# Optimization experiments

Measured on AMD Instinct MI355X. Metric: run time of the kernel, lower is better.

Reference implementation:

```python
import jax, jax.numpy as jnp
import numpy as np
import math

B, T, C = 2, 2048, 768
NH, HD = 12, 64  # n_head, head_dim

def setup_inputs() -> dict:
    key = jax.random.key(0)
    k1, k2, k3 = jax.random.split(key, 3)
    x = jax.random.normal(k1, (B, T, C), dtype=jnp.float32)
    mask = jnp.tril(jnp.ones((T, T), dtype=bool))[None, None]  # [1,1,T,T] causal
    Wqkv = jax.random.normal(k2, (C, 3 * C), dtype=jnp.float32) * (1.0 / math.sqrt(C))
    Wproj = jax.random.normal(k3, (C, C), dtype=jnp.float32) * (1.0 / math.sqrt(C))
    return {"x": x, "mask": mask, "Wqkv": Wqkv, "Wproj": Wproj}

def reference(x, mask, Wqkv, Wproj):
    b, t, c = x.shape
    qkv = x @ Wqkv  # [b,t,3c]
    q, k, v = jnp.split(qkv, 3, axis=-1)
    q = q.reshape(b, t, NH, HD).transpose(0, 2, 1, 3)  # [b,h,t,d]
    k = k.reshape(b, t, NH, HD).transpose(0, 2, 1, 3)
    v = v.reshape(b, t, NH, HD).transpose(0, 2, 1, 3)
    att = jnp.einsum('bhqd,bhkd->bhqk', q, k) / math.sqrt(HD)
    att = jnp.where(mask, att, -jnp.inf)
    att = jax.nn.softmax(att, axis=-1)
    out = jnp.einsum('bhqk,bhkd->bhqd', att, v)
    out = out.transpose(0, 2, 1, 3).reshape(b, t, c)
    return out @ Wproj
```

## Files before the change

### kernel.cpp

```cpp
#include <hip/hip_runtime.h>
#include <hip/hip_bf16.h>

#define T_   2048
#define C_   768
#define NH_  12
#define HD_  64
#define M_   (2*T_)
#define N1_  (3*C_)
#define PB_  ((size_t)NH_*T_*HD_)
#define KS_  0.180336880f
#define MK_  8.65617024f

typedef __attribute__((ext_vector_type(8))) short  short8;
typedef __attribute__((ext_vector_type(4))) short  shortx4;
typedef __attribute__((ext_vector_type(4))) float  floatx4;

__device__ __forceinline__ floatx4 mfma_bf16(short8 a, short8 b, floatx4 c) {
    return __builtin_amdgcn_mfma_f32_16x16x32_bf16(a, b, c, 0, 0, 0);
}
__device__ __forceinline__ float fast_exp2(float x) {
    return __builtin_amdgcn_exp2f(x);
}

__global__ __launch_bounds__(256) void prep1(const float* __restrict__ x,
                                             const float* __restrict__ wqkv,
                                             __hip_bfloat16* __restrict__ xb,
                                             __hip_bfloat16* __restrict__ wqkvT) {
    if (blockIdx.x < 3072) {
        const int idx = blockIdx.x * 256 + threadIdx.x;
        const floatx4 v = ((const floatx4*)x)[idx];
        union { __hip_bfloat16 h[4]; shortx4 s; } u;
#pragma unroll
        for (int j = 0; j < 4; j++) u.h[j] = __float2bfloat16(v[j]);
        ((shortx4*)xb)[idx] = u.s;
    } else {
        const int j  = (blockIdx.x - 3072) * 256 + threadIdx.x;
        const int k8 = j / N1_;
        const int n  = j - k8 * N1_;
        union { __hip_bfloat16 h[8]; short8 s; } u;
#pragma unroll
        for (int jj = 0; jj < 8; jj++)
            u.h[jj] = __float2bfloat16(wqkv[(size_t)(k8 * 8 + jj) * N1_ + n]);
        *(short8*)(wqkvT + (size_t)n * C_ + k8 * 8) = u.s;
    }
}

__global__ __launch_bounds__(256) void prep2(const float* __restrict__ wproj,
                                             __hip_bfloat16* __restrict__ wprojT) {
    const int j  = blockIdx.x * 256 + threadIdx.x;
    const int k8 = j / C_;
    const int n  = j - k8 * C_;
    union { __hip_bfloat16 h[8]; short8 s; } u;
#pragma unroll
    for (int jj = 0; jj < 8; jj++)
        u.h[jj] = __float2bfloat16(wproj[(size_t)(k8 * 8 + jj) * C_ + n]);
    *(short8*)(wprojT + (size_t)n * C_ + k8 * 8) = u.s;
}

__global__ __launch_bounds__(256) void gemm_bt128(const __hip_bfloat16* __restrict__ A,
                                                  const __hip_bfloat16* __restrict__ Bt,
                                                  int N, int K, int mode,
                                                  void* __restrict__ O0,
                                                  __hip_bfloat16* __restrict__ O1,
                                                  __hip_bfloat16* __restrict__ O2) {
    __shared__ __align__(16) __hip_bfloat16 As[128 * 40];
    __shared__ __align__(16) __hip_bfloat16 Bs[128 * 40];

    const int tid  = threadIdx.x;
    const int n0   = blockIdx.x * 128;
    const int m0   = blockIdx.y * 128;
    const int srow = tid >> 1;
    const int scol = (tid & 1) * 16;
    const int wave = tid >> 6;
    const int ln   = tid & 63;
    const int l16  = ln & 15;
    const int q4   = ln >> 4;
    const int wm   = (wave >> 1) * 64;
    const int wn   = (wave & 1) * 64;

    floatx4 acc[4][4];
#pragma unroll
    for (int i = 0; i < 4; i++)
#pragma unroll
        for (int j = 0; j < 4; j++) acc[i][j] = (floatx4){0.f, 0.f, 0.f, 0.f};

    const __hip_bfloat16* Ap = A  + (size_t)(m0 + srow) * K + scol;
    const __hip_bfloat16* Bp = Bt + (size_t)(n0 + srow) * K + scol;

    for (int k0 = 0; k0 < K; k0 += 32) {
        short8 a0 = *(const short8*)(Ap + k0);
        short8 a1 = *(const short8*)(Ap + k0 + 8);
        short8 b0 = *(const short8*)(Bp + k0);
        short8 b1 = *(const short8*)(Bp + k0 + 8);
        __syncthreads();
        *(short8*)(As + srow * 40 + scol)     = a0;
        *(short8*)(As + srow * 40 + scol + 8) = a1;
        *(short8*)(Bs + srow * 40 + scol)     = b0;
        *(short8*)(Bs + srow * 40 + scol + 8) = b1;
        __syncthreads();
        short8 af[4], bfr[4];
#pragma unroll
        for (int i = 0; i < 4; i++) {
            af[i]  = *(const short8*)(As + (wm + i * 16 + l16) * 40 + q4 * 8);
            bfr[i] = *(const short8*)(Bs + (wn + i * 16 + l16) * 40 + q4 * 8);
        }
#pragma unroll
        for (int i = 0; i < 4; i++)
#pragma unroll
            for (int j = 0; j < 4; j++)
                acc[i][j] = mfma_bf16(af[i], bfr[j], acc[i][j]);
    }

#pragma unroll
    for (int i = 0; i < 4; i++) {
        const int mbase = m0 + wm + i * 16 + q4 * 4;
#pragma unroll
        for (int j = 0; j < 4; j++) {
            const int n = n0 + wn + j * 16 + l16;
#pragma unroll
            for (int r = 0; r < 4; r++) {
                const int mm = mbase + r;
                const float fv = acc[i][j][r];
                if (mode == 1) {
                    ((float*)O0)[(size_t)mm * N + n] = fv;
                } else {
                    const __hip_bfloat16 hv = __float2bfloat16(fv);
                    const int which = n / C_;
                    const int rem   = n - which * C_;
                    const int h     = rem >> 6;
                    const int d     = rem & 63;
                    const int bh    = (mm >> 11) * NH_ + h;
                    const int t     = mm & (T_ - 1);
                    if (which == 0)      ((__hip_bfloat16*)O0)[((size_t)bh * T_ + t) * HD_ + d] = hv;
                    else if (which == 1) O1[((size_t)bh * T_ + t) * HD_ + d] = hv;
                    else                 O2[((size_t)bh * HD_ + d) * T_ + t] = hv;
                }
            }
        }
    }
}

__global__ __launch_bounds__(256) void gemm_bt64(const __hip_bfloat16* __restrict__ A,
                                                 const __hip_bfloat16* __restrict__ Bt,
                                                 int N, int K,
                                                 float* __restrict__ O0) {
    __shared__ __align__(16) __hip_bfloat16 As[64 * 40];
    __shared__ __align__(16) __hip_bfloat16 Bs[64 * 40];

    const int tid  = threadIdx.x;
    const int n0   = blockIdx.x * 64;
    const int m0   = blockIdx.y * 64;
    const int srow = tid >> 2;
    const int scol = (tid & 3) * 8;
    const int wave = tid >> 6;
    const int ln   = tid & 63;
    const int l16  = ln & 15;
    const int q4   = ln >> 4;
    const int wm   = (wave >> 1) * 32;
    const int wn   = (wave & 1) * 32;

    floatx4 acc[2][2];
#pragma unroll
    for (int i = 0; i < 2; i++)
#pragma unroll
        for (int j = 0; j < 2; j++) acc[i][j] = (floatx4){0.f, 0.f, 0.f, 0.f};

    const __hip_bfloat16* Ap = A  + (size_t)(m0 + srow) * K + scol;
    const __hip_bfloat16* Bp = Bt + (size_t)(n0 + srow) * K + scol;

    for (int k0 = 0; k0 < K; k0 += 32) {
        short8 av = *(const short8*)(Ap + k0);
        short8 bv = *(const short8*)(Bp + k0);
        __syncthreads();
        *(short8*)(As + srow * 40 + scol) = av;
        *(short8*)(Bs + srow * 40 + scol) = bv;
        __syncthreads();
        short8 af[2], bfr[2];
#pragma unroll
        for (int i = 0; i < 2; i++) {
            af[i]  = *(const short8*)(As + (wm + i * 16 + l16) * 40 + q4 * 8);
            bfr[i] = *(const short8*)(Bs + (wn + i * 16 + l16) * 40 + q4 * 8);
        }
#pragma unroll
        for (int i = 0; i < 2; i++)
#pragma unroll
            for (int j = 0; j < 2; j++)
                acc[i][j] = mfma_bf16(af[i], bfr[j], acc[i][j]);
    }

#pragma unroll
    for (int i = 0; i < 2; i++) {
        const int mbase = m0 + wm + i * 16 + q4 * 4;
#pragma unroll
        for (int j = 0; j < 2; j++) {
            const int n = n0 + wn + j * 16 + l16;
#pragma unroll
            for (int r = 0; r < 4; r++)
                O0[(size_t)(mbase + r) * N + n] = acc[i][j][r];
        }
    }
}

__global__ __launch_bounds__(256) void gemm_xw(const void* __restrict__ A,
                                               const float* __restrict__ Bf,
                                               int a_is_f32, int row0, int N, int K,
                                               int mode, int orow0,
                                               void* __restrict__ O0,
                                               __hip_bfloat16* __restrict__ O1,
                                               __hip_bfloat16* __restrict__ O2) {
    __shared__ __align__(16) __hip_bfloat16 As[128 * 40];
    __shared__ __align__(16) __hip_bfloat16 Bs[128 * 40];

    const int tid  = threadIdx.x;
    const int n0   = blockIdx.x * 128;
    const int m0   = blockIdx.y * 128;
    const int srow = tid >> 1;
    const int scol = (tid & 1) * 16;
    const int bn   = tid & 127;
    const int bg   = tid >> 7;
    const int wave = tid >> 6;
    const int ln   = tid & 63;
    const int l16  = ln & 15;
    const int q4   = ln >> 4;
    const int wm   = (wave >> 1) * 64;
    const int wn   = (wave & 1) * 64;

    floatx4 acc[4][4];
#pragma unroll
    for (int i = 0; i < 4; i++)
#pragma unroll
        for (int j = 0; j < 4; j++) acc[i][j] = (floatx4){0.f, 0.f, 0.f, 0.f};

    const size_t arow = (size_t)(row0 + m0 + srow) * K;

    for (int k0 = 0; k0 < K; k0 += 32) {
        union { __hip_bfloat16 h[16]; short8 v[2]; } au, bu;
        if (a_is_f32) {
            const float* Af = (const float*)A;
            const size_t base = arow + k0 + scol;
            floatx4 f0 = *(const floatx4*)(Af + base);
            floatx4 f1 = *(const floatx4*)(Af + base + 4);
            floatx4 f2 = *(const floatx4*)(Af + base + 8);
            floatx4 f3 = *(const floatx4*)(Af + base + 12);
#pragma unroll
            for (int j = 0; j < 4; j++) {
                au.h[j]      = __float2bfloat16(f0[j]);
                au.h[4 + j]  = __float2bfloat16(f1[j]);
                au.h[8 + j]  = __float2bfloat16(f2[j]);
                au.h[12 + j] = __float2bfloat16(f3[j]);
            }
        } else {
            const __hip_bfloat16* Ab = (const __hip_bfloat16*)A;
            au.v[0] = *(const short8*)(Ab + arow + k0 + scol);
            au.v[1] = *(const short8*)(Ab + arow + k0 + scol + 8);
        }
#pragma unroll
        for (int j = 0; j < 16; j++)
            bu.h[j] = __float2bfloat16(Bf[(size_t)(k0 + bg * 16 + j) * N + n0 + bn]);
        __syncthreads();
        *(short8*)(As + srow * 40 + scol)      = au.v[0];
        *(short8*)(As + srow * 40 + scol + 8)  = au.v[1];
        *(short8*)(Bs + bn * 40 + bg * 16)     = bu.v[0];
        *(short8*)(Bs + bn * 40 + bg * 16 + 8) = bu.v[1];
        __syncthreads();
        short8 af[4], bfr[4];
#pragma unroll
        for (int i = 0; i < 4; i++) {
            af[i]  = *(const short8*)(As + (wm + i * 16 + l16) * 40 + q4 * 8);
            bfr[i] = *(const short8*)(Bs + (wn + i * 16 + l16) * 40 + q4 * 8);
        }
#pragma unroll
        for (int i = 0; i < 4; i++)
#pragma unroll
            for (int j = 0; j < 4; j++)
                acc[i][j] = mfma_bf16(af[i], bfr[j], acc[i][j]);
    }

#pragma unroll
    for (int i = 0; i < 4; i++) {
        const int mbase = m0 + wm + i * 16 + q4 * 4;
#pragma unroll
        for (int j = 0; j < 4; j++) {
            const int n = n0 + wn + j * 16 + l16;
#pragma unroll
            for (int r = 0; r < 4; r++) {
                const int mm = mbase + r;
                const float fv = acc[i][j][r];
                if (mode == 1) {
                    ((float*)O0)[(size_t)(orow0 + mm) * N + n] = fv;
                } else {
                    const __hip_bfloat16 hv = __float2bfloat16(fv);
                    const int which = n / C_;
                    const int rem   = n - which * C_;
                    const int h     = rem >> 6;
                    const int d     = rem & 63;
                    const int bh    = (mm >> 11) * NH_ + h;
                    const int t     = mm & (T_ - 1);
                    if (which == 0)      ((__hip_bfloat16*)O0)[((size_t)bh * T_ + t) * HD_ + d] = hv;
                    else if (which == 1) O1[((size_t)bh * T_ + t) * HD_ + d] = hv;
                    else                 O2[((size_t)bh * HD_ + d) * T_ + t] = hv;
                }
            }
        }
    }
}

__global__ __launch_bounds__(256) void attn_fused(const __hip_bfloat16* __restrict__ Q,
                                                  const __hip_bfloat16* __restrict__ Kd,
                                                  const __hip_bfloat16* __restrict__ Vt,
                                                  __hip_bfloat16* __restrict__ O) {
    __shared__ __align__(16) __hip_bfloat16 plds[4][2][16][72];

    const int bh   = blockIdx.x;
    const int wid  = threadIdx.x >> 6;
    const int lane = threadIdx.x & 63;
    const int l16  = lane & 15;
    const int q4   = lane >> 4;
    const int i    = 63 - (int)blockIdx.y;
    const int q0A  = 32 * i;
    const int q0B  = 32 * i + 16;
    const int nch  = (i >> 1) + 1;

    const __hip_bfloat16* Qh = Q  + (size_t)bh * T_ * HD_;
    const __hip_bfloat16* Kh = Kd + (size_t)bh * T_ * HD_;
    const __hip_bfloat16* Vh = Vt + (size_t)bh * HD_ * T_;

    short8 aqA[2], aqB[2];
#pragma unroll
    for (int kt = 0; kt < 2; kt++) {
        aqA[kt] = *(const short8*)(Qh + (size_t)(q0A + l16) * HD_ + kt * 32 + q4 * 8);
        aqB[kt] = *(const short8*)(Qh + (size_t)(q0B + l16) * HD_ + kt * 32 + q4 * 8);
    }

    floatx4 accA[4], accB[4];
#pragma unroll
    for (int ct = 0; ct < 4; ct++) {
        accA[ct] = (floatx4){0.f, 0.f, 0.f, 0.f};
        accB[ct] = (floatx4){0.f, 0.f, 0.f, 0.f};
    }
    float lsA[4] = {0.f, 0.f, 0.f, 0.f};
    float lsB[4] = {0.f, 0.f, 0.f, 0.f};

    for (int c = wid; c < nch; c += 4) {
        const int kv0 = c * 64;
        const bool diag = (c == nch - 1);

        short8 bk[4][2];
#pragma unroll
        for (int nt = 0; nt < 4; nt++)
#pragma unroll
            for (int kt = 0; kt < 2; kt++)
                bk[nt][kt] = *(const short8*)(Kh + (size_t)(kv0 + nt * 16 + l16) * HD_ + kt * 32 + q4 * 8);

        floatx4 sA[4], sB[4];
#pragma unroll
        for (int nt = 0; nt < 4; nt++) {
            sA[nt] = (floatx4){0.f, 0.f, 0.f, 0.f};
            sB[nt] = (floatx4){0.f, 0.f, 0.f, 0.f};
#pragma unroll
            for (int kt = 0; kt < 2; kt++) {
                sA[nt] = mfma_bf16(aqA[kt], bk[nt][kt], sA[nt]);
                sB[nt] = mfma_bf16(aqB[kt], bk[nt][kt], sB[nt]);
            }
        }

        if (diag) {
#pragma unroll
            for (int r = 0; r < 4; r++) {
#pragma unroll
                for (int nt = 0; nt < 4; nt++) {
                    const int kvc = kv0 + nt * 16 + l16;
                    if (kvc > q0A + q4 * 4 + r) sA[nt][r] = -3e38f;
                    if (kvc > q0B + q4 * 4 + r) sB[nt][r] = -3e38f;
                }
            }
        }

#pragma unroll
        for (int r = 0; r < 4; r++) {
            float ra = 0.f, rb = 0.f;
#pragma unroll
            for (int nt = 0; nt < 4; nt++) {
                const float pa = fast_exp2(sA[nt][r] * KS_ - MK_);
                const float pb = fast_exp2(sB[nt][r] * KS_ - MK_);
                plds[wid][0][q4 * 4 + r][nt * 16 + l16] = __float2bfloat16(pa);
                plds[wid][1][q4 * 4 + r][nt * 16 + l16] = __float2bfloat16(pb);
                ra += pa; rb += pb;
            }
            lsA[r] += ra; lsB[r] += rb;
        }

        __threadfence_block();

        short8 apA[2], apB[2];
#pragma unroll
        for (int kt = 0; kt < 2; kt++) {
            apA[kt] = *(const short8*)(&plds[wid][0][l16][kt * 32 + q4 * 8]);
            apB[kt] = *(const short8*)(&plds[wid][1][l16][kt * 32 + q4 * 8]);
        }
#pragma unroll
        for (int ct = 0; ct < 4; ct++)
#pragma unroll
            for (int kt = 0; kt < 2; kt++) {
                short8 bv = *(const short8*)(Vh + (size_t)(ct * 16 + l16) * T_ + kv0 + kt * 32 + q4 * 8);
                accA[ct] = mfma_bf16(apA[kt], bv, accA[ct]);
                accB[ct] = mfma_bf16(apB[kt], bv, accB[ct]);
            }

        __threadfence_block();
    }

#pragma unroll
    for (int off = 1; off < 16; off <<= 1)
#pragma unroll
        for (int r = 0; r < 4; r++) {
            lsA[r] += __shfl_xor(lsA[r], off, 64);
            lsB[r] += __shfl_xor(lsB[r], off, 64);
        }

    __syncthreads();
    floatx4* accbuf = (floatx4*)&plds[0][0][0][0];
    float*   lbuf   = (float*)((char*)&plds[0][0][0][0] + 16384);

    auto publish = [&](int slot) {
#pragma unroll
        for (int ct = 0; ct < 4; ct++) {
            accbuf[((slot * 2 + 0) * 4 + ct) * 64 + lane] = accA[ct];
            accbuf[((slot * 2 + 1) * 4 + ct) * 64 + lane] = accB[ct];
        }
        if (l16 == 0) {
#pragma unroll
            for (int r = 0; r < 4; r++) {
                lbuf[(slot * 2 + 0) * 16 + q4 * 4 + r] = lsA[r];
                lbuf[(slot * 2 + 1) * 16 + q4 * 4 + r] = lsB[r];
            }
        }
    };
    auto mergeIn = [&](int slot) {
#pragma unroll
        for (int ct = 0; ct < 4; ct++) {
            accA[ct] += accbuf[((slot * 2 + 0) * 4 + ct) * 64 + lane];
            accB[ct] += accbuf[((slot * 2 + 1) * 4 + ct) * 64 + lane];
        }
#pragma unroll
        for (int r = 0; r < 4; r++) {
            lsA[r] += lbuf[(slot * 2 + 0) * 16 + q4 * 4 + r];
            lsB[r] += lbuf[(slot * 2 + 1) * 16 + q4 * 4 + r];
        }
    };

    if (wid >= 2) publish(wid - 2);
    __syncthreads();
    if (wid < 2) mergeIn(wid);
    __syncthreads();
    if (wid == 1) publish(0);
    __syncthreads();
    if (wid == 0) {
        mergeIn(0);
        const int orow0 = (bh / NH_) * T_;
        const int hcol  = (bh % NH_) * HD_;
#pragma unroll
        for (int r = 0; r < 4; r++) {
            const float invA = 1.0f / lsA[r];
            const float invB = 1.0f / lsB[r];
            __hip_bfloat16* oA = O + (size_t)(orow0 + q0A + q4 * 4 + r) * C_ + hcol;
            __hip_bfloat16* oB = O + (size_t)(orow0 + q0B + q4 * 4 + r) * C_ + hcol;
#pragma unroll
            for (int ct = 0; ct < 4; ct++) {
                oA[ct * 16 + l16] = __float2bfloat16(accA[ct][r] * invA);
                oB[ct * 16 + l16] = __float2bfloat16(accB[ct][r] * invB);
            }
        }
    }
}

extern "C" void kernel_launch(void* const* d_in, const int* in_sizes, int n_in,
                              void* d_out, int out_size, void* d_ws, size_t ws_size,
                              hipStream_t stream) {
    const float *x = nullptr, *wqkv = nullptr, *wproj = nullptr;
    for (int i = 0; i < n_in; i++) {
        const int s = in_sizes[i];
        if (s == M_ * C_ && !x) x = (const float*)d_in[i];
        else if (s == C_ * N1_ && !wqkv) wqkv = (const float*)d_in[i];
        else if (s == C_ * C_ && !wproj) wproj = (const float*)d_in[i];
    }
    float* out = (float*)d_out;
    __hip_bfloat16* ws = (__hip_bfloat16*)d_ws;
    __hip_bfloat16* Vt = (__hip_bfloat16*)d_out;

    const size_t needB = 6 * PB_ * 2;
    if (ws_size >= needB) {
        __hip_bfloat16* Qall   = ws;
        __hip_bfloat16* Kall   = Qall + 2 * PB_;
        __hip_bfloat16* ATT    = Kall + 2 * PB_;
        __hip_bfloat16* xb     = ATT;
        __hip_bfloat16* wqkvT  = (__hip_bfloat16*)d_out + 2 * PB_;
        __hip_bfloat16* wprojT = Qall;
        prep1<<<dim3(3936), 256, 0, stream>>>(x, wqkv, xb, wqkvT);
        gemm_bt128<<<dim3(N1_ / 128, M_ / 128), 256, 0, stream>>>(
            xb, wqkvT, N1_, C_, 0, (void*)Qall, Kall, Vt);
        attn_fused<<<dim3(2 * NH_, 64), 256, 0, stream>>>(Qall, Kall, Vt, ATT);
        prep2<<<dim3(288), 256, 0, stream>>>(wproj, wprojT);
        gemm_bt64<<<dim3(C_ / 64, M_ / 64), 256, 0, stream>>>(ATT, wprojT, C_, C_, out);
    } else {
        __hip_bfloat16* Qb      = ws;
        __hip_bfloat16* Kb      = Qb + PB_;
        __hip_bfloat16* ATTb[2] = {Kb + PB_, Kb + 2 * PB_};
        for (int b = 0; b < 2; b++) {
            __hip_bfloat16* Vtb = Vt + (size_t)b * PB_;
            gemm_xw<<<dim3(N1_ / 128, T_ / 128), 256, 0, stream>>>(
                x, wqkv, 1, b * T_, N1_, C_, 0, 0, (void*)Qb, Kb, Vtb);
            attn_fused<<<dim3(NH_, 64), 256, 0, stream>>>(Qb, Kb, Vtb, ATTb[b]);
        }
        for (int b = 0; b < 2; b++)
            gemm_xw<<<dim3(C_ / 128, T_ / 128), 256, 0, stream>>>(
                ATTb[b], wproj, 0, 0, C_, C_, 1, b * T_, (void*)out, nullptr, nullptr);
    }
}
```

Baseline: 206.1 us.

## Pair causal query tiles per attention block to balance work across blocks

```diff
diff --git a/kernel.cpp b/kernel.cpp
--- a/kernel.cpp
+++ b/kernel.cpp
@@ -20,6 +20,9 @@
 }
 __device__ __forceinline__ float fast_exp2(float x) {
     return __builtin_amdgcn_exp2f(x);
+}
+__device__ __forceinline__ void wave_fence() {
+    __builtin_amdgcn_fence(__ATOMIC_SEQ_CST, "wavefront");
 }
 
 __global__ __launch_bounds__(256) void prep1(const float* __restrict__ x,
@@ -201,179 +204,83 @@
     }
 }
 
-__global__ __launch_bounds__(256) void gemm_xw(const void* __restrict__ A,
-                                               const float* __restrict__ Bf,
-                                               int a_is_f32, int row0, int N, int K,
-                                               int mode, int orow0,
-                                               void* __restrict__ O0,
-                                               __hip_bfloat16* __restrict__ O1,
-                                               __hip_bfloat16* __restrict__ O2) {
-    __shared__ __align__(16) __hip_bfloat16 As[128 * 40];
-    __shared__ __align__(16) __hip_bfloat16 Bs[128 * 40];
-
-    const int tid  = threadIdx.x;
-    const int n0   = blockIdx.x * 128;
-    const int m0   = blockIdx.y * 128;
-    const int srow = tid >> 1;
-    const int scol = (tid & 1) * 16;
-    const int bn   = tid & 127;
-    const int bg   = tid >> 7;
-    const int wave = tid >> 6;
-    const int ln   = tid & 63;
-    const int l16  = ln & 15;
-    const int q4   = ln >> 4;
-    const int wm   = (wave >> 1) * 64;
-    const int wn   = (wave & 1) * 64;
-
-    floatx4 acc[4][4];
-#pragma unroll
-    for (int i = 0; i < 4; i++)
-#pragma unroll
-        for (int j = 0; j < 4; j++) acc[i][j] = (floatx4){0.f, 0.f, 0.f, 0.f};
-
-    const size_t arow = (size_t)(row0 + m0 + srow) * K;
-
-    for (int k0 = 0; k0 < K; k0 += 32) {
-        union { __hip_bfloat16 h[16]; short8 v[2]; } au, bu;
-        if (a_is_f32) {
-            const float* Af = (const float*)A;
-            const size_t base = arow + k0 + scol;
-            floatx4 f0 = *(const floatx4*)(Af + base);
-            floatx4 f1 = *(const floatx4*)(Af + base + 4);
-            floatx4 f2 = *(const floatx4*)(Af + base + 8);
-            floatx4 f3 = *(const floatx4*)(Af + base + 12);
-#pragma unroll
-            for (int j = 0; j < 4; j++) {
-                au.h[j]      = __float2bfloat16(f0[j]);
-                au.h[4 + j]  = __float2bfloat16(f1[j]);
-                au.h[8 + j]  = __float2bfloat16(f2[j]);
-                au.h[12 + j] = __float2bfloat16(f3[j]);
-            }
-        } else {
-            const __hip_bfloat16* Ab = (const __hip_bfloat16*)A;
-            au.v[0] = *(const short8*)(Ab + arow + k0 + scol);
-            au.v[1] = *(const short8*)(Ab + arow + k0 + scol + 8);
-        }
-#pragma unroll
-        for (int j = 0; j < 16; j++)
-            bu.h[j] = __float2bfloat16(Bf[(size_t)(k0 + bg * 16 + j) * N + n0 + bn]);
-        __syncthreads();
-        *(short8*)(As + srow * 40 + scol)      = au.v[0];
-        *(short8*)(As + srow * 40 + scol + 8)  = au.v[1];
-        *(short8*)(Bs + bn * 40 + bg * 16)     = bu.v[0];
-        *(short8*)(Bs + bn * 40 + bg * 16 + 8) = bu.v[1];
-        __syncthreads();
-        short8 af[4], bfr[4];
-#pragma unroll
-        for (int i = 0; i < 4; i++) {
-            af[i]  = *(const short8*)(As + (wm + i * 16 + l16) * 40 + q4 * 8);
-            bfr[i] = *(const short8*)(Bs + (wn + i * 16 + l16) * 40 + q4 * 8);
-        }
-#pragma unroll
-        for (int i = 0; i < 4; i++)
-#pragma unroll
-            for (int j = 0; j < 4; j++)
-                acc[i][j] = mfma_bf16(af[i], bfr[j], acc[i][j]);
-    }
-
-#pragma unroll
-    for (int i = 0; i < 4; i++) {
-        const int mbase = m0 + wm + i * 16 + q4 * 4;
-#pragma unroll
-        for (int j = 0; j < 4; j++) {
-            const int n = n0 + wn + j * 16 + l16;
-#pragma unroll
-            for (int r = 0; r < 4; r++) {
-                const int mm = mbase + r;
-                const float fv = acc[i][j][r];
-                if (mode == 1) {
-                    ((float*)O0)[(size_t)(orow0 + mm) * N + n] = fv;
-                } else {
-                    const __hip_bfloat16 hv = __float2bfloat16(fv);
-                    const int which = n / C_;
-                    const int rem   = n - which * C_;
-                    const int h     = rem >> 6;
-                    const int d     = rem & 63;
-                    const int bh    = (mm >> 11) * NH_ + h;
-                    const int t     = mm & (T_ - 1);
-                    if (which == 0)      ((__hip_bfloat16*)O0)[((size_t)bh * T_ + t) * HD_ + d] = hv;
-                    else if (which == 1) O1[((size_t)bh * T_ + t) * HD_ + d] = hv;
-                    else                 O2[((size_t)bh * HD_ + d) * T_ + t] = hv;
-                }
-            }
-        }
-    }
-}
-
 __global__ __launch_bounds__(256) void attn_fused(const __hip_bfloat16* __restrict__ Q,
                                                   const __hip_bfloat16* __restrict__ Kd,
                                                   const __hip_bfloat16* __restrict__ Vt,
                                                   __hip_bfloat16* __restrict__ O) {
-    __shared__ __align__(16) __hip_bfloat16 plds[4][2][16][72];
+    __shared__ __align__(16) char smem[33792];
 
     const int bh   = blockIdx.x;
+    const int j    = blockIdx.y;
     const int wid  = threadIdx.x >> 6;
     const int lane = threadIdx.x & 63;
     const int l16  = lane & 15;
     const int q4   = lane >> 4;
-    const int i    = 63 - (int)blockIdx.y;
-    const int q0A  = 32 * i;
-    const int q0B  = 32 * i + 16;
-    const int nch  = (i >> 1) + 1;
+    const int i0   = j;
+    const int i1   = 63 - j;
+    const int nch0 = (i0 >> 1) + 1;
+    const int nch1 = (i1 >> 1) + 1;
+    const int q0[4] = {32 * i0, 32 * i0 + 16, 32 * i1, 32 * i1 + 16};
+
+    auto plds = (__hip_bfloat16(*)[2][16][72])smem;
 
     const __hip_bfloat16* Qh = Q  + (size_t)bh * T_ * HD_;
     const __hip_bfloat16* Kh = Kd + (size_t)bh * T_ * HD_;
     const __hip_bfloat16* Vh = Vt + (size_t)bh * HD_ * T_;
 
-    short8 aqA[2], aqB[2];
-#pragma unroll
-    for (int kt = 0; kt < 2; kt++) {
-        aqA[kt] = *(const short8*)(Qh + (size_t)(q0A + l16) * HD_ + kt * 32 + q4 * 8);
-        aqB[kt] = *(const short8*)(Qh + (size_t)(q0B + l16) * HD_ + kt * 32 + q4 * 8);
-    }
-
-    floatx4 accA[4], accB[4];
+    short8 aq[4][2];
+#pragma unroll
+    for (int t = 0; t < 4; t++)
+#pragma unroll
+        for (int kt = 0; kt < 2; kt++)
+            aq[t][kt] = *(const short8*)(Qh + (size_t)(q0[t] + l16) * HD_ + kt * 32 + q4 * 8);
+
+    floatx4 acc0A[4], acc0B[4], acc1A[4], acc1B[4];
 #pragma unroll
     for (int ct = 0; ct < 4; ct++) {
-        accA[ct] = (floatx4){0.f, 0.f, 0.f, 0.f};
-        accB[ct] = (floatx4){0.f, 0.f, 0.f, 0.f};
-    }
-    float lsA[4] = {0.f, 0.f, 0.f, 0.f};
-    float lsB[4] = {0.f, 0.f, 0.f, 0.f};
-
-    for (int c = wid; c < nch; c += 4) {
-        const int kv0 = c * 64;
-        const bool diag = (c == nch - 1);
-
-        short8 bk[4][2];
-#pragma unroll
-        for (int nt = 0; nt < 4; nt++)
-#pragma unroll
-            for (int kt = 0; kt < 2; kt++)
-                bk[nt][kt] = *(const short8*)(Kh + (size_t)(kv0 + nt * 16 + l16) * HD_ + kt * 32 + q4 * 8);
-
+        acc0A[ct] = (floatx4){0.f, 0.f, 0.f, 0.f};
+        acc0B[ct] = (floatx4){0.f, 0.f, 0.f, 0.f};
+        acc1A[ct] = (floatx4){0.f, 0.f, 0.f, 0.f};
+        acc1B[ct] = (floatx4){0.f, 0.f, 0.f, 0.f};
+    }
+    float ls[4][4];
+#pragma unroll
+    for (int t = 0; t < 4; t++)
+#pragma unroll
+        for (int r = 0; r < 4; r++) ls[t][r] = 0.f;
+
+    auto do_chunk = [&](int kv0, bool diag, int q0A, int q0B,
+                        short8 (&aqA)[2], short8 (&aqB)[2],
+                        floatx4 (&accA)[4], floatx4 (&accB)[4],
+                        float (&lsA)[4], float (&lsB)[4]) {
         floatx4 sA[4], sB[4];
 #pragma unroll
         for (int nt = 0; nt < 4; nt++) {
             sA[nt] = (floatx4){0.f, 0.f, 0.f, 0.f};
             sB[nt] = (floatx4){0.f, 0.f, 0.f, 0.f};
-#pragma unroll
-            for (int kt = 0; kt < 2; kt++) {
-                sA[nt] = mfma_bf16(aqA[kt], bk[nt][kt], sA[nt]);
-                sB[nt] = mfma_bf16(aqB[kt], bk[nt][kt], sB[nt]);
+        }
+#pragma unroll
+        for (int kt = 0; kt < 2; kt++) {
+            short8 bk[4];
+#pragma unroll
+            for (int nt = 0; nt < 4; nt++)
+                bk[nt] = *(const short8*)(Kh + (size_t)(kv0 + nt * 16 + l16) * HD_ + kt * 32 + q4 * 8);
+#pragma unroll
+            for (int nt = 0; nt < 4; nt++) {
+                sA[nt] = mfma_bf16(aqA[kt], bk[nt], sA[nt]);
+                sB[nt] = mfma_bf16(aqB[kt], bk[nt], sB[nt]);
             }
         }
 
         if (diag) {
 #pragma unroll
-            for (int r = 0; r < 4; r++) {
+            for (int r = 0; r < 4; r++)
 #pragma unroll
                 for (int nt = 0; nt < 4; nt++) {
                     const int kvc = kv0 + nt * 16 + l16;
                     if (kvc > q0A + q4 * 4 + r) sA[nt][r] = -3e38f;
                     if (kvc > q0B + q4 * 4 + r) sB[nt][r] = -3e38f;
                 }
-            }
         }
 
 #pragma unroll
@@ -390,7 +297,7 @@
             lsA[r] += ra; lsB[r] += rb;
         }
 
-        __threadfence_block();
+        wave_fence();
 
         short8 apA[2], apB[2];
 #pragma unroll
@@ -407,45 +314,55 @@
                 accB[ct] = mfma_bf16(apB[kt], bv, accB[ct]);
             }
 
-        __threadfence_block();
+        wave_fence();
+    };
+
+    for (int t = wid; t < 33; t += 4) {
+        if (t < nch0) {
+            do_chunk(t * 64, t == nch0 - 1, q0[0], q0[1], aq[0], aq[1],
+                     acc0A, acc0B, ls[0], ls[1]);
+        } else {
+            const int c = t - nch0;
+            do_chunk(c * 64, c == nch1 - 1, q0[2], q0[3], aq[2], aq[3],
+                     acc1A, acc1B, ls[2], ls[3]);
+        }
     }
 
 #pragma unroll
     for (int off = 1; off < 16; off <<= 1)
 #pragma unroll
-        for (int r = 0; r < 4; r++) {
-            lsA[r] += __shfl_xor(lsA[r], off, 64);
-            lsB[r] += __shfl_xor(lsB[r], off, 64);
-        }
+        for (int t = 0; t < 4; t++)
+#pragma unroll
+            for (int r = 0; r < 4; r++)
+                ls[t][r] += __shfl_xor(ls[t][r], off, 64);
 
     __syncthreads();
-    floatx4* accbuf = (floatx4*)&plds[0][0][0][0];
-    float*   lbuf   = (float*)((char*)&plds[0][0][0][0] + 16384);
+    floatx4* accbuf = (floatx4*)smem;
+    float*   lbuf   = (float*)(smem + 32768);
 
     auto publish = [&](int slot) {
-#pragma unroll
-        for (int ct = 0; ct < 4; ct++) {
-            accbuf[((slot * 2 + 0) * 4 + ct) * 64 + lane] = accA[ct];
-            accbuf[((slot * 2 + 1) * 4 + ct) * 64 + lane] = accB[ct];
-        }
-        if (l16 == 0) {
-#pragma unroll
-            for (int r = 0; r < 4; r++) {
-                lbuf[(slot * 2 + 0) * 16 + q4 * 4 + r] = lsA[r];
-                lbuf[(slot * 2 + 1) * 16 + q4 * 4 + r] = lsB[r];
-            }
+        floatx4* a[4] = {acc0A, acc0B, acc1A, acc1B};
+#pragma unroll
+        for (int t = 0; t < 4; t++) {
+#pragma unroll
+            for (int ct = 0; ct < 4; ct++)
+                accbuf[(((slot * 4 + t) * 4) + ct) * 64 + lane] = a[t][ct];
+            if (l16 == 0)
+#pragma unroll
+                for (int r = 0; r < 4; r++)
+                    lbuf[(slot * 4 + t) * 16 + q4 * 4 + r] = ls[t][r];
         }
     };
     auto mergeIn = [&](int slot) {
-#pragma unroll
-        for (int ct = 0; ct < 4; ct++) {
-            accA[ct] += accbuf[((slot * 2 + 0) * 4 + ct) * 64 + lane];
-            accB[ct] += accbuf[((slot * 2 + 1) * 4 + ct) * 64 + lane];
-        }
-#pragma unroll
-        for (int r = 0; r < 4; r++) {
-            lsA[r] += lbuf[(slot * 2 + 0) * 16 + q4 * 4 + r];
-            lsB[r] += lbuf[(slot * 2 + 1) * 16 + q4 * 4 + r];
+        floatx4* a[4] = {acc0A, acc0B, acc1A, acc1B};
+#pragma unroll
+        for (int t = 0; t < 4; t++) {
+#pragma unroll
+            for (int ct = 0; ct < 4; ct++)
+                a[t][ct] += accbuf[(((slot * 4 + t) * 4) + ct) * 64 + lane];
+#pragma unroll
+            for (int r = 0; r < 4; r++)
+                ls[t][r] += lbuf[(slot * 4 + t) * 16 + q4 * 4 + r];
         }
     };
 
@@ -459,18 +376,17 @@
         mergeIn(0);
         const int orow0 = (bh / NH_) * T_;
         const int hcol  = (bh % NH_) * HD_;
-#pragma unroll
-        for (int r = 0; r < 4; r++) {
-            const float invA = 1.0f / lsA[r];
-            const float invB = 1.0f / lsB[r];
-            __hip_bfloat16* oA = O + (size_t)(orow0 + q0A + q4 * 4 + r) * C_ + hcol;
-            __hip_bfloat16* oB = O + (size_t)(orow0 + q0B + q4 * 4 + r) * C_ + hcol;
-#pragma unroll
-            for (int ct = 0; ct < 4; ct++) {
-                oA[ct * 16 + l16] = __float2bfloat16(accA[ct][r] * invA);
-                oB[ct * 16 + l16] = __float2bfloat16(accB[ct][r] * invB);
+        floatx4* a[4] = {acc0A, acc0B, acc1A, acc1B};
+#pragma unroll
+        for (int t = 0; t < 4; t++)
+#pragma unroll
+            for (int r = 0; r < 4; r++) {
+                const float inv = 1.0f / ls[t][r];
+                __hip_bfloat16* orow = O + (size_t)(orow0 + q0[t] + q4 * 4 + r) * C_ + hcol;
+#pragma unroll
+                for (int ct = 0; ct < 4; ct++)
+                    orow[ct * 16 + l16] = __float2bfloat16(a[t][ct][r] * inv);
             }
-        }
     }
 }
 
@@ -488,32 +404,16 @@
     __hip_bfloat16* ws = (__hip_bfloat16*)d_ws;
     __hip_bfloat16* Vt = (__hip_bfloat16*)d_out;
 
-    const size_t needB = 6 * PB_ * 2;
-    if (ws_size >= needB) {
-        __hip_bfloat16* Qall   = ws;
-        __hip_bfloat16* Kall   = Qall + 2 * PB_;
-        __hip_bfloat16* ATT    = Kall + 2 * PB_;
-        __hip_bfloat16* xb     = ATT;
-        __hip_bfloat16* wqkvT  = (__hip_bfloat16*)d_out + 2 * PB_;
-        __hip_bfloat16* wprojT = Qall;
-        prep1<<<dim3(3936), 256, 0, stream>>>(x, wqkv, xb, wqkvT);
-        gemm_bt128<<<dim3(N1_ / 128, M_ / 128), 256, 0, stream>>>(
-            xb, wqkvT, N1_, C_, 0, (void*)Qall, Kall, Vt);
-        attn_fused<<<dim3(2 * NH_, 64), 256, 0, stream>>>(Qall, Kall, Vt, ATT);
-        prep2<<<dim3(288), 256, 0, stream>>>(wproj, wprojT);
-        gemm_bt64<<<dim3(C_ / 64, M_ / 64), 256, 0, stream>>>(ATT, wprojT, C_, C_, out);
-    } else {
-        __hip_bfloat16* Qb      = ws;
-        __hip_bfloat16* Kb      = Qb + PB_;
-        __hip_bfloat16* ATTb[2] = {Kb + PB_, Kb + 2 * PB_};
-        for (int b = 0; b < 2; b++) {
-            __hip_bfloat16* Vtb = Vt + (size_t)b * PB_;
-            gemm_xw<<<dim3(N1_ / 128, T_ / 128), 256, 0, stream>>>(
-                x, wqkv, 1, b * T_, N1_, C_, 0, 0, (void*)Qb, Kb, Vtb);
-            attn_fused<<<dim3(NH_, 64), 256, 0, stream>>>(Qb, Kb, Vtb, ATTb[b]);
-        }
-        for (int b = 0; b < 2; b++)
-            gemm_xw<<<dim3(C_ / 128, T_ / 128), 256, 0, stream>>>(
-                ATTb[b], wproj, 0, 0, C_, C_, 1, b * T_, (void*)out, nullptr, nullptr);
-    }
-}
+    __hip_bfloat16* Qall   = ws;
+    __hip_bfloat16* Kall   = Qall + 2 * PB_;
+    __hip_bfloat16* ATT    = Kall + 2 * PB_;
+    __hip_bfloat16* xb     = ATT;
+    __hip_bfloat16* wqkvT  = (__hip_bfloat16*)d_out + 2 * PB_;
+    __hip_bfloat16* wprojT = Qall;
+    prep1<<<dim3(3936), 256, 0, stream>>>(x, wqkv, xb, wqkvT);
+    gemm_bt128<<<dim3(N1_ / 128, M_ / 128), 256, 0, stream>>>(
+        xb, wqkvT, N1_, C_, 0, (void*)Qall, Kall, Vt);
+    attn_fused<<<dim3(2 * NH_, 32), 256, 0, stream>>>(Qall, Kall, Vt, ATT);
+    prep2<<<dim3(288), 256, 0, stream>>>(wproj, wprojT);
+    gemm_bt64<<<dim3(C_ / 64, M_ / 64), 256, 0, stream>>>(ATT, wprojT, C_, C_, out);
+}
```

Measured after the change: 226.8 us. 1.1x slower.
